# Optimization experiments

Measured on AMD Instinct MI355X. Metric: run time of the kernel, lower is better.

## Reference

```python
import jax, jax.numpy as jnp
import numpy as np


def _lsap_np(cost):
    """Jonker-Volgenant / Hungarian (e-maxx formulation) for a square cost
    matrix. Returns col_of_row: row i is assigned to column col_of_row[i].
    Matches scipy.optimize.linear_sum_assignment on square matrices."""
    cost = np.asarray(cost, dtype=np.float64)
    n = cost.shape[0]
    u = np.zeros(n + 1)
    v = np.zeros(n + 1)
    p = np.zeros(n + 1, dtype=np.int64)   # p[j] = row assigned to column j (1-based; 0 = none)
    way = np.zeros(n + 1, dtype=np.int64)
    for i in range(1, n + 1):
        p[0] = i
        j0 = 0
        minv = np.full(n + 1, np.inf)
        used = np.zeros(n + 1, dtype=bool)
        while True:
            used[j0] = True
            i0 = p[j0]
            js = np.nonzero(~used[1:])[0] + 1  # unused columns (vectorized inner loop)
            cur = cost[i0 - 1, js - 1] - u[i0] - v[js]
            better = cur < minv[js]
            minv[js] = np.where(better, cur, minv[js])
            way[js] = np.where(better, j0, way[js])
            j1 = js[np.argmin(minv[js])]
            delta = minv[j1]
            u[p[used]] += delta          # rows assigned to used columns are distinct
            v[used] -= delta
            minv[~used] -= delta
            j0 = j1
            if p[j0] == 0:
                break
        # augment along the alternating path
        while j0 != 0:
            j1 = way[j0]
            p[j0] = p[j1]
            j0 = j1
    col_of_row = np.zeros(n, dtype=np.int32)
    for j in range(1, n + 1):
        if p[j] > 0:
            col_of_row[p[j] - 1] = j - 1
    return col_of_row


def _batched_lsap_host(dists):
    dists = np.asarray(dists)
    return np.stack([_lsap_np(d) for d in dists]).astype(np.int32)  # [B, N]


def _pairwise_dist(y_true, y_pred):
    # dist[b, i, j] = || y_true[b, i] - y_pred[b, j] ||_2, matching tf.norm(..., axis=-1)
    diff = y_true[:, :, None, :] - y_pred[:, None, :, :]  # [B, N, N, D]
    return jnp.sqrt(jnp.sum(diff * diff, axis=-1))        # [B, N, N]


def setup_inputs() -> dict:
    key = jax.random.key(0)
    k1, k2 = jax.random.split(key)
    B, N, D = 64, 128, 64
    y_true = jax.random.normal(k1, (B, N, D), dtype=jnp.float32)
    y_pred = jax.random.normal(k2, (B, N, D), dtype=jnp.float32)
    return {"y_true": y_true, "y_pred": y_pred}


def reference(y_true, y_pred):
    dist = _pairwise_dist(y_true, y_pred)                      # [B, N, N]
    B, N = dist.shape[0], dist.shape[1]
    col_ind = jax.pure_callback(
        _batched_lsap_host,
        jax.ShapeDtypeStruct((B, N), jnp.int32),
        jax.lax.stop_gradient(dist),
    )                                                          # [B, N]
    matched = jnp.take_along_axis(dist, col_ind[:, :, None].astype(jnp.int32), axis=2)[..., 0]
    batch_losses = jnp.sum(matched, axis=1)                    # [B]
    return jnp.mean(batch_losses)
```

## Files before the change

kernel.cpp:

```cpp
#include <hip/hip_runtime.h>
#include <math.h>
#include <stdint.h>

#define BATCH 64
#define N 128
#define DIM 64
#define ARR_CAP 640

typedef unsigned uint32x2_t __attribute__((ext_vector_type(2)));

__device__ __forceinline__ unsigned monokey(float x) {
    unsigned b = __float_as_uint(x);
    return b ^ (unsigned)(((int)b >> 31) | (int)0x80000000u);
}

__device__ __forceinline__ unsigned umin_(unsigned a, unsigned b) { return a < b ? a : b; }
__device__ __forceinline__ unsigned umax_(unsigned a, unsigned b) { return a > b ? a : b; }
__device__ __forceinline__ int rfl(int v) { return __builtin_amdgcn_readfirstlane(v); }
__device__ __forceinline__ int rl_i(int v, int l) { return __builtin_amdgcn_readlane(v, l); }
__device__ __forceinline__ float rl_f(float v, int l) {
    return __int_as_float(__builtin_amdgcn_readlane(__float_as_int(v), l));
}

#define DPP_ROR(x, n) __builtin_amdgcn_update_dpp((int)(x), (int)(x), 0x120 + (n), 0xF, 0xF, false)

__device__ __forceinline__ unsigned wave_kmin(unsigned k) {
    unsigned a = (unsigned)DPP_ROR(k, 1);
    unsigned b = (unsigned)DPP_ROR(k, 2);
    k = umin_(k, umin_(a, b));
    a = (unsigned)DPP_ROR(k, 3);
    b = (unsigned)DPP_ROR(k, 6);
    k = umin_(k, umin_(a, b));
    a = (unsigned)DPP_ROR(k, 9);
    k = umin_(k, a);
#if __has_builtin(__builtin_amdgcn_permlane16_swap)
    {
        uint32x2_t r = __builtin_amdgcn_permlane16_swap(k, k, false, false);
        k = umin_(r[0], r[1]);
    }
#else
    k = umin_(k, (unsigned)__shfl_xor((int)k, 16));
#endif
#if __has_builtin(__builtin_amdgcn_permlane32_swap)
    {
        uint32x2_t r = __builtin_amdgcn_permlane32_swap(k, k, false, false);
        k = umin_(r[0], r[1]);
    }
#else
    k = umin_(k, (unsigned)__shfl_xor((int)k, 32));
#endif
    return k;
}

__device__ __forceinline__ void wave_kmin2(unsigned& ks, unsigned& kb, int lane) {
    unsigned ps, pb;
#define KM2_COMBINE { unsigned ns = umin_(ks, ps); kb = umin_(umin_(kb, pb), umax_(ks, ps)); ks = ns; }
    ps = (unsigned)DPP_ROR(ks, 1); pb = (unsigned)DPP_ROR(kb, 1); KM2_COMBINE;
    ps = (unsigned)DPP_ROR(ks, 2); pb = (unsigned)DPP_ROR(kb, 2); KM2_COMBINE;
    ps = (unsigned)DPP_ROR(ks, 4); pb = (unsigned)DPP_ROR(kb, 4); KM2_COMBINE;
    ps = (unsigned)DPP_ROR(ks, 8); pb = (unsigned)DPP_ROR(kb, 8); KM2_COMBINE;
#if __has_builtin(__builtin_amdgcn_permlane16_swap)
    {
        uint32x2_t rs = __builtin_amdgcn_permlane16_swap(ks, ks, false, false);
        uint32x2_t rb = __builtin_amdgcn_permlane16_swap(kb, kb, false, false);
        ps = (lane & 16) ? rs[0] : rs[1]; pb = (lane & 16) ? rb[0] : rb[1];
    }
    KM2_COMBINE;
#else
    ps = (unsigned)__shfl_xor((int)ks, 16); pb = (unsigned)__shfl_xor((int)kb, 16); KM2_COMBINE;
#endif
#if __has_builtin(__builtin_amdgcn_permlane32_swap)
    {
        uint32x2_t rs = __builtin_amdgcn_permlane32_swap(ks, ks, false, false);
        uint32x2_t rb = __builtin_amdgcn_permlane32_swap(kb, kb, false, false);
        ps = (lane & 32) ? rs[0] : rs[1]; pb = (lane & 32) ? rb[0] : rb[1];
    }
    KM2_COMBINE;
#else
    ps = (unsigned)__shfl_xor((int)ks, 32); pb = (unsigned)__shfl_xor((int)kb, 32); KM2_COMBINE;
#endif
#undef KM2_COMBINE
}

#define PACK_KEY(val, p, colbit, lane) \
    ((monokey(val) & 0xFFFF8000u) | ((unsigned)(p) << 7) | ((unsigned)(colbit) << 6) | (unsigned)(lane))

__global__ __launch_bounds__(64, 1)
void lsap_kernel(const float* __restrict__ y_true, const float* __restrict__ y_pred,
                 float* __restrict__ batch_sums, float* __restrict__ out, int use_atomic) {
    __shared__ float dist[N * N];
    __shared__ float ytl[N * DIM];
    __shared__ int unlist[N + 8];
    __shared__ int flags[N];

    const int b = blockIdx.x;
    const int lane = threadIdx.x;
    const int ca = lane, cb = lane + 64;
    const int ja = lane + 1, jb = lane + 65;

    {
        const float4* yt4 = (const float4*)(y_true + (size_t)b * N * DIM);
        float4* ytl4 = (float4*)ytl;
        for (int k = lane; k < N * DIM / 4; k += 64) ytl4[k] = yt4[k];
    }

    float ypa[DIM], ypb[DIM];
    {
        const float4* pa4 = (const float4*)(y_pred + (size_t)b * N * DIM + (size_t)ca * DIM);
        const float4* pb4 = (const float4*)(y_pred + (size_t)b * N * DIM + (size_t)cb * DIM);
        #pragma unroll
        for (int k = 0; k < DIM / 4; ++k) {
            float4 v4 = pa4[k];
            ypa[4*k+0]=v4.x; ypa[4*k+1]=v4.y; ypa[4*k+2]=v4.z; ypa[4*k+3]=v4.w;
            float4 w4 = pb4[k];
            ypb[4*k+0]=w4.x; ypb[4*k+1]=w4.y; ypb[4*k+2]=w4.z; ypb[4*k+3]=w4.w;
        }
    }
    __syncthreads();

    float va = INFINITY, vb = INFINITY;
    for (int i = 0; i < N; ++i) {
        const float4* yr = (const float4*)(ytl + i * DIM);
        float a0 = 0.f, a1 = 0.f;
        #pragma unroll
        for (int k = 0; k < DIM / 4; ++k) {
            float4 t4 = yr[k];
            float d;
            d = t4.x - ypa[4*k+0]; a0 = fmaf(d, d, a0);
            d = t4.y - ypa[4*k+1]; a0 = fmaf(d, d, a0);
            d = t4.z - ypa[4*k+2]; a0 = fmaf(d, d, a0);
            d = t4.w - ypa[4*k+3]; a0 = fmaf(d, d, a0);
            d = t4.x - ypb[4*k+0]; a1 = fmaf(d, d, a1);
            d = t4.y - ypb[4*k+1]; a1 = fmaf(d, d, a1);
            d = t4.z - ypb[4*k+2]; a1 = fmaf(d, d, a1);
            d = t4.w - ypb[4*k+3]; a1 = fmaf(d, d, a1);
        }
        float d0 = sqrtf(a0), d1 = sqrtf(a1);
        dist[i * N + ca] = d0;
        dist[i * N + cb] = d1;
        va = fminf(va, d0);
        vb = fminf(vb, d1);
    }

    int   pa = 0, pb = 0;
    float upa = 0.f, upb = 0.f;
    float ura = 0.f, urb = 0.f;
    int   waya = 0, wayb = 0;

    int nun = 0;
    float pd0 = dist[ca], pd1 = dist[cb];
    for (int r = 0; r < N; ++r) {
        float c0 = pd0 - va, c1 = pd1 - vb;
        if (r + 1 < N) { pd0 = dist[(r+1) * N + ca]; pd1 = dist[(r+1) * N + cb]; }
        unsigned k0 = PACK_KEY(c0, pa, 0, lane);
        unsigned k1 = PACK_KEY(c1, pb, 1, lane);
        unsigned ks = umin_(k0, k1), kb2 = umax_(k0, k1);
        wave_kmin2(ks, kb2, lane);
        int s1 = rfl((int)ks);
        int s2 = rfl((int)kb2);
        int w1 = s1 & 63, cb1 = (s1 >> 6) & 1, pj1 = (s1 >> 7) & 0xFF;
        float u1 = rl_f(cb1 ? c1 : c0, w1);
        float u2 = rl_f(((s2 >> 6) & 1) ? c1 : c0, s2 & 63);
        int j1 = 1 + w1 + (cb1 << 6);
        if (pj1 == 0) {
            float dd = u2 - u1;
            if (ja == j1) { pa = r + 1; upa = u2; va -= dd; }
            if (jb == j1) { pb = r + 1; upb = u2; vb -= dd; }
            if ((r & 63) == lane) { if (r < 64) ura = u2; else urb = u2; }
        } else {
            unlist[nun] = r;
            ++nun;
            if ((r & 63) == lane) { if (r < 64) ura = u1; else urb = u1; }
        }
    }

    {
        int k = 0;
        int icur = -1; float d0 = 0.f, d1 = 0.f;
        int qi = -1; float qd0 = 0.f, qd1 = 0.f;
        if (nun > 0) {
            icur = rfl(unlist[0]); k = 1;
            d0 = dist[icur * N + ca]; d1 = dist[icur * N + cb];
            if (k < nun) { qi = rfl(unlist[k]); qd0 = dist[qi * N + ca]; qd1 = dist[qi * N + cb]; }
        }
        int ops = 0;
        while (icur >= 0 && ops < ARR_CAP) {
            ++ops;
            float c0 = d0 - va, c1 = d1 - vb;
            unsigned k0 = PACK_KEY(c0, pa, 0, lane);
            unsigned k1 = PACK_KEY(c1, pb, 1, lane);
            unsigned ks = umin_(k0, k1), kb2 = umax_(k0, k1);
            wave_kmin2(ks, kb2, lane);
            int s1 = rfl((int)ks);
            int s2 = rfl((int)kb2);
            int pj1 = (s1 >> 7) & 0xFF, pj2 = (s2 >> 7) & 0xFF;
            bool transfer = ((unsigned)s1 >> 15) < ((unsigned)s2 >> 15);
            int it0 = transfer ? pj1 : (pj1 ? pj2 : 0);

            float nd0, nd1;
            if (it0) { nd0 = dist[(it0 - 1) * N + ca]; nd1 = dist[(it0 - 1) * N + cb]; }
            else     { nd0 = qd0; nd1 = qd1; }

            int w1 = s1 & 63, cb1 = (s1 >> 6) & 1;
            int w2 = s2 & 63, cb2 = (s2 >> 6) & 1;
            float u1 = rl_f(cb1 ? c1 : c0, w1);
            float u2 = rl_f(cb2 ? c1 : c0, w2);
            int j1 = 1 + w1 + (cb1 << 6);
            int j2 = 1 + w2 + (cb2 << 6);
            int jt = transfer ? j1 : (pj1 ? j2 : j1);
            if (transfer) {
                float dd = u2 - u1;
                if (ja == j1) va -= dd;
                if (jb == j1) vb -= dd;
            }
            if (ja == jt) { pa = icur + 1; upa = u2; }
            if (jb == jt) { pb = icur + 1; upb = u2; }
            if ((icur & 63) == lane) { if (icur < 64) ura = u2; else urb = u2; }

            if (it0) { icur = it0 - 1; d0 = nd0; d1 = nd1; }
            else {
                icur = qi; d0 = nd0; d1 = nd1;
                if (icur >= 0) {
                    ++k;
                    if (k < nun) { qi = rfl(unlist[k]); qd0 = dist[qi * N + ca]; qd1 = dist[qi * N + cb]; }
                    else qi = -1;
                }
            }
        }
    }

    flags[lane] = 0; flags[lane + 64] = 0;
    if (pa) flags[pa - 1] = 1;
    if (pb) flags[pb - 1] = 1;
    int f0 = flags[lane] ^ 1;
    int f1 = flags[lane + 64] ^ 1;
    unsigned long long b0 = __ballot(f0), b1 = __ballot(f1);
    int nfree0 = __popcll(b0);
    int nfree = nfree0 + __popcll(b1);
    unsigned long long lt = (1ull << lane) - 1ull;
    if (f0) unlist[__popcll(b0 & lt)] = lane;
    if (f1) unlist[nfree0 + __popcll(b1 & lt)] = lane + 64;

    for (int t = 0; t < nfree; ++t) {
        int r = rfl(unlist[t]);
        float d0 = dist[r * N + ca], d1 = dist[r * N + cb];
        float u_i = rl_f((r >= 64) ? urb : ura, r & 63);
        float mina = INFINITY, minb = INFINITY;
        int useda = 0, usedb = 0;
        waya = 0; wayb = 0;
        float uacca = 0.f, uaccb = 0.f;
        float u_acc_i = u_i;
        float u0c = u_i;
        int j0 = 0;

        for (int it = 0; it < 2 * N; ++it) {
            if (ja == j0) useda = 1;
            if (jb == j0) usedb = 1;
            if (!useda) { float cur = d0 - u0c - va; if (cur < mina) { mina = cur; waya = j0; } }
            if (!usedb) { float cur = d1 - u0c - vb; if (cur < minb) { minb = cur; wayb = j0; } }

            float fa = useda ? INFINITY : mina;
            float fb = usedb ? INFINITY : minb;
            unsigned kA = PACK_KEY(fa, pa, 0, lane);
            unsigned kB = PACK_KEY(fb, pb, 1, lane);
            unsigned kk = wave_kmin(umin_(kA, kB));
            int s = rfl((int)kk);
            int i1 = (s >> 7) & 0xFF;

            float nd0, nd1;
            if (i1) { nd0 = dist[(i1 - 1) * N + ca]; nd1 = dist[(i1 - 1) * N + cb]; }

            int w = s & 63, cbw = (s >> 6) & 1;
            float delta = rl_f(cbw ? fb : fa, w);
            float u1v = rl_f(cbw ? upb : upa, w);

            if (useda) { va -= delta; uacca += delta; } else { mina -= delta; }
            if (usedb) { vb -= delta; uaccb += delta; } else { minb -= delta; }
            u_acc_i += delta;

            j0 = 1 + w + (cbw << 6);
            if (i1 == 0) break;
            u0c = u1v; d0 = nd0; d1 = nd1;
        }

        if (useda) upa += uacca;
        if (usedb) upb += uaccb;

        int jj = j0;
        for (int hop = 0; hop < N + 1; ++hop) {
            int wj = (jj - 1) & 63;
            int sbj = (jj > 64) ? 1 : 0;
            int jp = rl_i(sbj ? wayb : waya, wj);
            int np; float nu;
            if (jp == 0) { np = r + 1; nu = u_acc_i; }
            else {
                int wp = (jp - 1) & 63;
                int sbp = (jp > 64) ? 1 : 0;
                np = rl_i(sbp ? pb : pa, wp);
                nu = rl_f(sbp ? upb : upa, wp);
            }
            if (ja == jj) { pa = np; upa = nu; }
            if (jb == jj) { pb = np; upb = nu; }
            if (jp == 0) break;
            jj = jp;
        }
    }

    float s = dist[(pa - 1) * N + ca] + dist[(pb - 1) * N + cb];
    #pragma unroll
    for (int m = 1; m < 64; m <<= 1) s += __shfl_xor(s, m);
    if (lane == 0) {
        if (use_atomic) atomicAdd(out, s * (1.0f / (float)BATCH));
        else batch_sums[b] = s;
    }
}

__global__ __launch_bounds__(64)
void reduce_kernel(const float* __restrict__ bs, float* __restrict__ out) {
    int tid = threadIdx.x;
    float v = bs[tid];
    #pragma unroll
    for (int m = 1; m < 64; m <<= 1) v += __shfl_xor(v, m);
    if (tid == 0) out[0] = v * (1.0f / (float)BATCH);
}

extern "C" void kernel_launch(void* const* d_in, const int* in_sizes, int n_in,
                              void* d_out, int out_size, void* d_ws, size_t ws_size,
                              hipStream_t stream) {
    const float* y_true = (const float*)d_in[0];
    const float* y_pred = (const float*)d_in[1];
    float* out = (float*)d_out;

    if (ws_size >= BATCH * sizeof(float)) {
        float* bs = (float*)d_ws;
        lsap_kernel<<<BATCH, 64, 0, stream>>>(y_true, y_pred, bs, out, 0);
        reduce_kernel<<<1, 64, 0, stream>>>(bs, out);
    } else {
        hipMemsetAsync(d_out, 0, sizeof(float), stream);
        lsap_kernel<<<BATCH, 64, 0, stream>>>(y_true, y_pred, nullptr, out, 1);
    }
}
```

Baseline: 701.7 us.

## Use full-precision keys in init and auction phases, queue displaced rows for reuse

The column-reduction and augmenting-row-reduction phases now pack only the cost and lane index into the min key, keeping nearly all mantissa bits. The row index is fetched with a readlane instead of being packed into the key. The transfer test now compares the exact float minima. When a row is displaced in the ARR phase it is appended to the unassigned queue instead of being dropped, so the free-row list comes straight from the queue and the flags/ballot pass is removed. This aims for more exact ARR decisions so fewer rows fall through to the costly shortest-augmenting-path phase, at the price of extra readlanes and speculative LDS loads for both candidate rows on each iteration.

```diff
diff --git a/kernel.cpp b/kernel.cpp
--- a/kernel.cpp
+++ b/kernel.cpp
@@ -34,18 +34,12 @@
     a = (unsigned)DPP_ROR(k, 9);
     k = umin_(k, a);
 #if __has_builtin(__builtin_amdgcn_permlane16_swap)
-    {
-        uint32x2_t r = __builtin_amdgcn_permlane16_swap(k, k, false, false);
-        k = umin_(r[0], r[1]);
-    }
+    { uint32x2_t r = __builtin_amdgcn_permlane16_swap(k, k, false, false); k = umin_(r[0], r[1]); }
 #else
     k = umin_(k, (unsigned)__shfl_xor((int)k, 16));
 #endif
 #if __has_builtin(__builtin_amdgcn_permlane32_swap)
-    {
-        uint32x2_t r = __builtin_amdgcn_permlane32_swap(k, k, false, false);
-        k = umin_(r[0], r[1]);
-    }
+    { uint32x2_t r = __builtin_amdgcn_permlane32_swap(k, k, false, false); k = umin_(r[0], r[1]); }
 #else
     k = umin_(k, (unsigned)__shfl_xor((int)k, 32));
 #endif
@@ -82,16 +76,12 @@
 #undef KM2_COMBINE
 }
 
-#define PACK_KEY(val, p, colbit, lane) \
-    ((monokey(val) & 0xFFFF8000u) | ((unsigned)(p) << 7) | ((unsigned)(colbit) << 6) | (unsigned)(lane))
-
 __global__ __launch_bounds__(64, 1)
 void lsap_kernel(const float* __restrict__ y_true, const float* __restrict__ y_pred,
                  float* __restrict__ batch_sums, float* __restrict__ out, int use_atomic) {
     __shared__ float dist[N * N];
     __shared__ float ytl[N * DIM];
-    __shared__ int unlist[N + 8];
-    __shared__ int flags[N];
+    __shared__ int unlist[N + ARR_CAP + 8];
 
     const int b = blockIdx.x;
     const int lane = threadIdx.x;
@@ -152,16 +142,17 @@
     for (int r = 0; r < N; ++r) {
         float c0 = pd0 - va, c1 = pd1 - vb;
         if (r + 1 < N) { pd0 = dist[(r+1) * N + ca]; pd1 = dist[(r+1) * N + cb]; }
-        unsigned k0 = PACK_KEY(c0, pa, 0, lane);
-        unsigned k1 = PACK_KEY(c1, pb, 1, lane);
+        unsigned k0 = (monokey(c0) & ~0x7Fu) | (unsigned)lane;
+        unsigned k1 = (monokey(c1) & ~0x7Fu) | 64u | (unsigned)lane;
         unsigned ks = umin_(k0, k1), kb2 = umax_(k0, k1);
         wave_kmin2(ks, kb2, lane);
         int s1 = rfl((int)ks);
         int s2 = rfl((int)kb2);
-        int w1 = s1 & 63, cb1 = (s1 >> 6) & 1, pj1 = (s1 >> 7) & 0xFF;
+        int w1 = s1 & 63, cb1 = (s1 >> 6) & 1;
         float u1 = rl_f(cb1 ? c1 : c0, w1);
         float u2 = rl_f(((s2 >> 6) & 1) ? c1 : c0, s2 & 63);
         int j1 = 1 + w1 + (cb1 << 6);
+        int pj1 = rl_i(cb1 ? pb : pa, w1);
         if (pj1 == 0) {
             float dd = u2 - u1;
             if (ja == j1) { pa = r + 1; upa = u2; va -= dd; }
@@ -174,74 +165,70 @@
         }
     }
 
-    {
-        int k = 0;
-        int icur = -1; float d0 = 0.f, d1 = 0.f;
+    int qk = 0, nf = nun;
+    {
+        int ops = 0;
+        int icur = -1;
+        float d0c = 0.f, d1c = 0.f;
         int qi = -1; float qd0 = 0.f, qd1 = 0.f;
         if (nun > 0) {
-            icur = rfl(unlist[0]); k = 1;
-            d0 = dist[icur * N + ca]; d1 = dist[icur * N + cb];
-            if (k < nun) { qi = rfl(unlist[k]); qd0 = dist[qi * N + ca]; qd1 = dist[qi * N + cb]; }
-        }
-        int ops = 0;
+            icur = rfl(unlist[0]); qk = 1;
+            d0c = dist[icur * N + ca]; d1c = dist[icur * N + cb];
+            if (qk < nf) { qi = rfl(unlist[qk]); qd0 = dist[qi * N + ca]; qd1 = dist[qi * N + cb]; }
+        }
         while (icur >= 0 && ops < ARR_CAP) {
             ++ops;
-            float c0 = d0 - va, c1 = d1 - vb;
-            unsigned k0 = PACK_KEY(c0, pa, 0, lane);
-            unsigned k1 = PACK_KEY(c1, pb, 1, lane);
+            float c0 = d0c - va, c1 = d1c - vb;
+            unsigned k0 = (monokey(c0) & ~0x7Fu) | (unsigned)lane;
+            unsigned k1 = (monokey(c1) & ~0x7Fu) | 64u | (unsigned)lane;
             unsigned ks = umin_(k0, k1), kb2 = umax_(k0, k1);
             wave_kmin2(ks, kb2, lane);
             int s1 = rfl((int)ks);
             int s2 = rfl((int)kb2);
-            int pj1 = (s1 >> 7) & 0xFF, pj2 = (s2 >> 7) & 0xFF;
-            bool transfer = ((unsigned)s1 >> 15) < ((unsigned)s2 >> 15);
-            int it0 = transfer ? pj1 : (pj1 ? pj2 : 0);
-
-            float nd0, nd1;
-            if (it0) { nd0 = dist[(it0 - 1) * N + ca]; nd1 = dist[(it0 - 1) * N + cb]; }
-            else     { nd0 = qd0; nd1 = qd1; }
-
             int w1 = s1 & 63, cb1 = (s1 >> 6) & 1;
             int w2 = s2 & 63, cb2 = (s2 >> 6) & 1;
+            int pj1 = rl_i(cb1 ? pb : pa, w1);
+            int pj2 = rl_i(cb2 ? pb : pa, w2);
+            float sa0 = 0.f, sa1 = 0.f, sb0 = 0.f, sb1 = 0.f;
+            if (pj1) { sa0 = dist[(pj1 - 1) * N + ca]; sa1 = dist[(pj1 - 1) * N + cb]; }
+            if (pj2) { sb0 = dist[(pj2 - 1) * N + ca]; sb1 = dist[(pj2 - 1) * N + cb]; }
             float u1 = rl_f(cb1 ? c1 : c0, w1);
             float u2 = rl_f(cb2 ? c1 : c0, w2);
             int j1 = 1 + w1 + (cb1 << 6);
             int j2 = 1 + w2 + (cb2 << 6);
-            int jt = transfer ? j1 : (pj1 ? j2 : j1);
+            bool transfer = (u1 < u2);
+            int jt, it0;
             if (transfer) {
                 float dd = u2 - u1;
                 if (ja == j1) va -= dd;
                 if (jb == j1) vb -= dd;
-            }
+                jt = j1; it0 = pj1;
+            } else if (pj1 > 0) { jt = j2; it0 = pj2; }
+            else { jt = j1; it0 = 0; }
+
             if (ja == jt) { pa = icur + 1; upa = u2; }
             if (jb == jt) { pb = icur + 1; upb = u2; }
             if ((icur & 63) == lane) { if (icur < 64) ura = u2; else urb = u2; }
 
-            if (it0) { icur = it0 - 1; d0 = nd0; d1 = nd1; }
-            else {
-                icur = qi; d0 = nd0; d1 = nd1;
-                if (icur >= 0) {
-                    ++k;
-                    if (k < nun) { qi = rfl(unlist[k]); qd0 = dist[qi * N + ca]; qd1 = dist[qi * N + cb]; }
-                    else qi = -1;
-                }
+            if (transfer && it0 > 0) {
+                icur = it0 - 1; d0c = sa0; d1c = sa1;
+            } else {
+                if (!transfer && pj1 > 0) { unlist[nf] = it0 - 1; ++nf; }
+                if (qk < nf) {
+                    if (qi < 0) { icur = it0 - 1; d0c = sb0; d1c = sb1; }
+                    else        { icur = qi;      d0c = qd0; d1c = qd1; }
+                    ++qk;
+                    if (qk < nf) {
+                        qi = rfl(unlist[qk]);
+                        qd0 = dist[qi * N + ca]; qd1 = dist[qi * N + cb];
+                    } else qi = -1;
+                } else icur = -1;
             }
         }
-    }
-
-    flags[lane] = 0; flags[lane + 64] = 0;
-    if (pa) flags[pa - 1] = 1;
-    if (pb) flags[pb - 1] = 1;
-    int f0 = flags[lane] ^ 1;
-    int f1 = flags[lane + 64] ^ 1;
-    unsigned long long b0 = __ballot(f0), b1 = __ballot(f1);
-    int nfree0 = __popcll(b0);
-    int nfree = nfree0 + __popcll(b1);
-    unsigned long long lt = (1ull << lane) - 1ull;
-    if (f0) unlist[__popcll(b0 & lt)] = lane;
-    if (f1) unlist[nfree0 + __popcll(b1 & lt)] = lane + 64;
-
-    for (int t = 0; t < nfree; ++t) {
+        if (icur >= 0) { --qk; unlist[qk] = icur; }
+    }
+
+    for (int t = qk; t < nf; ++t) {
         int r = rfl(unlist[t]);
         float d0 = dist[r * N + ca], d1 = dist[r * N + cb];
         float u_i = rl_f((r >= 64) ? urb : ura, r & 63);
@@ -259,19 +246,19 @@
             if (!useda) { float cur = d0 - u0c - va; if (cur < mina) { mina = cur; waya = j0; } }
             if (!usedb) { float cur = d1 - u0c - vb; if (cur < minb) { minb = cur; wayb = j0; } }
 
-            float fa = useda ? INFINITY : mina;
-            float fb = usedb ? INFINITY : minb;
-            unsigned kA = PACK_KEY(fa, pa, 0, lane);
-            unsigned kB = PACK_KEY(fb, pb, 1, lane);
+            float fa_ = useda ? INFINITY : mina;
+            float fb_ = usedb ? INFINITY : minb;
+            unsigned kA = (monokey(fa_) & 0xFFFF8000u) | ((unsigned)pa << 7) | (unsigned)lane;
+            unsigned kB = (monokey(fb_) & 0xFFFF8000u) | ((unsigned)pb << 7) | 64u | (unsigned)lane;
             unsigned kk = wave_kmin(umin_(kA, kB));
             int s = rfl((int)kk);
             int i1 = (s >> 7) & 0xFF;
 
-            float nd0, nd1;
+            float nd0 = 0.f, nd1 = 0.f;
             if (i1) { nd0 = dist[(i1 - 1) * N + ca]; nd1 = dist[(i1 - 1) * N + cb]; }
 
             int w = s & 63, cbw = (s >> 6) & 1;
-            float delta = rl_f(cbw ? fb : fa, w);
+            float delta = rl_f(cbw ? fb_ : fa_, w);
             float u1v = rl_f(cbw ? upb : upa, w);
 
             if (useda) { va -= delta; uacca += delta; } else { mina -= delta; }
```

Measured after the change: 592.4 us. 1.18x faster.
